# Kernel optimization log

Hardware: AMD Instinct MI355X
Metric: run time of the kernel (lower is better)

The kernel has to match this reference:

```python
import jax, jax.numpy as jnp
import numpy as np

UNITS = 32
ATT_WIDTH = 64


def setup_inputs() -> dict:
    key = jax.random.key(0)
    ks = jax.random.split(key, 4)
    B, T, F = 4, 1024, 256
    x = jax.random.normal(ks[0], (B, T, F), dtype=jnp.float32)
    Wt = jax.random.normal(ks[1], (F, UNITS), dtype=jnp.float32) * (1.0 / np.sqrt(F))
    Wx = jax.random.normal(ks[2], (F, UNITS), dtype=jnp.float32) * (1.0 / np.sqrt(F))
    bh = jnp.zeros((UNITS,), dtype=jnp.float32)
    Wa = jax.random.normal(ks[3], (UNITS, 1), dtype=jnp.float32) * (1.0 / np.sqrt(UNITS))
    ba = jnp.zeros((1,), dtype=jnp.float32)
    return {"x": x, "Wt": Wt, "Wx": Wx, "bh": bh, "Wa": Wa, "ba": ba}


def reference(x, Wt, Wx, bh, Wa, ba):
    # Additive (Bahdanau-style) self-attention emission:
    # h[b,t,s,u] = tanh(x[b,t] @ Wt + x[b,s] @ Wx + bh)
    q = jnp.einsum('btf,fu->btu', x, Wt)[:, :, None, :]   # [B,T,1,U]
    k = jnp.einsum('bsf,fu->bsu', x, Wx)[:, None, :, :]   # [B,1,T,U]
    h = jnp.tanh(q + k + bh)                               # [B,T,T,U]
    e = jnp.einsum('btsu,uo->bts', h, Wa) + ba[0]          # [B,T,T]

    # Local attention window (symmetric, width=ATT_WIDTH)
    T = x.shape[1]
    idx = jnp.arange(T)
    lower = idx - ATT_WIDTH // 2                           # [T]
    band = (lower[:, None] <= idx[None, :]) & (idx[None, :] < lower[:, None] + ATT_WIDTH)
    e = e - 10000.0 * (1.0 - band.astype(e.dtype))

    a = jax.nn.softmax(e, axis=-1)                         # [B,T,T]
    v = jnp.einsum('bts,bsf->btf', a, x)                   # [B,T,F]
    return v
```

## Files before the change

kernel.cpp:

```cpp
#include <hip/hip_runtime.h>
#include <math.h>

#define BB 4
#define TT 1024
#define FF 256
#define UU 32
#define HALF_W 32
#define WMAX 64

__device__ __forceinline__ float fast_tanh(float x) {
    float e = __expf(2.0f * x);
    return 1.0f - 2.0f / (e + 1.0f);
}

__global__ __launch_bounds__(256) void qk_kernel(
    const float* __restrict__ x, const float* __restrict__ Wt,
    const float* __restrict__ Wx, const float* __restrict__ bh,
    float* __restrict__ qbuf, float* __restrict__ kbuf) {
    int row0 = blockIdx.x * 4;
    int tid = threadIdx.x;
    __shared__ float xs[4][FF];
    {
        int r = tid >> 6;
        int c4 = tid & 63;
        ((float4*)xs[r])[c4] = ((const float4*)(x + (size_t)(row0 + r) * FF))[c4];
    }
    __syncthreads();
    int r = tid >> 6;
    int half = (tid >> 5) & 1;
    int u = tid & 31;
    const float* __restrict__ W = half ? Wx : Wt;
    const float* __restrict__ xr = xs[r];
    float acc = 0.f;
#pragma unroll 8
    for (int f = 0; f < FF; ++f)
        acc = fmaf(xr[f], W[f * UU + u], acc);
    int row = row0 + r;
    if (half == 0) qbuf[row * UU + u] = acc + bh[u];
    else           kbuf[row * UU + u] = acc;
}

__global__ __launch_bounds__(256) void attn_kernel(
    const float* __restrict__ x, const float* __restrict__ qbuf,
    const float* __restrict__ kbuf, const float* __restrict__ Wa,
    const float* __restrict__ ba, float* __restrict__ out) {
    int row = blockIdx.x;
    int t = row & (TT - 1);
    int b = row >> 10;
    int tid = threadIdx.x;
    int s0 = max(0, t - HALF_W);
    int s1 = min(TT, t + HALF_W);
    int W_ = s1 - s0;

    __shared__ float q_sh[UU];
    __shared__ float wa_sh[UU];
    __shared__ float e_sh[WMAX];
    __shared__ float a_sh[WMAX];

    if (tid < UU) {
        q_sh[tid]  = qbuf[row * UU + tid];
        wa_sh[tid] = Wa[tid];
    }
    __syncthreads();

    int sl = tid >> 2;
    int j  = tid & 3;
    float partial = 0.f;
    if (sl < W_) {
        const float4* krow = (const float4*)(kbuf + (size_t)(b * TT + s0 + sl) * UU + j * 8);
        float4 k0 = krow[0];
        float4 k1 = krow[1];
        int u = j * 8;
        partial  = fast_tanh(q_sh[u + 0] + k0.x) * wa_sh[u + 0];
        partial += fast_tanh(q_sh[u + 1] + k0.y) * wa_sh[u + 1];
        partial += fast_tanh(q_sh[u + 2] + k0.z) * wa_sh[u + 2];
        partial += fast_tanh(q_sh[u + 3] + k0.w) * wa_sh[u + 3];
        partial += fast_tanh(q_sh[u + 4] + k1.x) * wa_sh[u + 4];
        partial += fast_tanh(q_sh[u + 5] + k1.y) * wa_sh[u + 5];
        partial += fast_tanh(q_sh[u + 6] + k1.z) * wa_sh[u + 6];
        partial += fast_tanh(q_sh[u + 7] + k1.w) * wa_sh[u + 7];
    }
    partial += __shfl_xor(partial, 1);
    partial += __shfl_xor(partial, 2);
    if (j == 0) e_sh[sl] = (sl < W_) ? partial + ba[0] : -1e30f;
    __syncthreads();

    if (tid < 64) {
        float e = e_sh[tid];
        float m = e;
#pragma unroll
        for (int off = 1; off < 64; off <<= 1) m = fmaxf(m, __shfl_xor(m, off));
        float p = __expf(e - m);
        float sum = p;
#pragma unroll
        for (int off = 1; off < 64; off <<= 1) sum += __shfl_xor(sum, off);
        a_sh[tid] = p / sum;
    }
    __syncthreads();

    float acc = 0.f;
    const float* xb = x + (size_t)(b * TT + s0) * FF + tid;
#pragma unroll 4
    for (int k2 = 0; k2 < W_; ++k2)
        acc = fmaf(a_sh[k2], xb[(size_t)k2 * FF], acc);
    out[(size_t)row * FF + tid] = acc;
}

__global__ __launch_bounds__(256) void fused_kernel(
    const float* __restrict__ x, const float* __restrict__ Wt,
    const float* __restrict__ Wx, const float* __restrict__ bh,
    const float* __restrict__ Wa, const float* __restrict__ ba,
    float* __restrict__ out) {
    int row = blockIdx.x;
    int t = row & (TT - 1);
    int b = row >> 10;
    int tid = threadIdx.x;
    int s0 = max(0, t - HALF_W);
    int s1 = min(TT, t + HALF_W);
    int W_ = s1 - s0;

    __shared__ float ks[WMAX * UU];
    __shared__ float q_sh[UU];
    __shared__ float wa_sh[UU];
    __shared__ float e_sh[WMAX];
    __shared__ float a_sh[WMAX];

    if (tid < UU) {
        const float* xr = x + (size_t)row * FF;
        float acc = 0.f;
        for (int f = 0; f < FF; ++f) acc = fmaf(xr[f], Wt[f * UU + tid], acc);
        q_sh[tid]  = acc + bh[tid];
        wa_sh[tid] = Wa[tid];
    }
    for (int p = tid; p < W_ * UU; p += 256) {
        int sl = p >> 5, u = p & 31;
        const float* xr = x + (size_t)(b * TT + s0 + sl) * FF;
        float acc = 0.f;
        for (int f = 0; f < FF; ++f) acc = fmaf(xr[f], Wx[f * UU + u], acc);
        ks[p] = acc;
    }
    __syncthreads();

    int sl = tid >> 2;
    int j  = tid & 3;
    float partial = 0.f;
    if (sl < W_) {
#pragma unroll
        for (int uu = 0; uu < 8; ++uu) {
            int u = j * 8 + uu;
            partial += fast_tanh(q_sh[u] + ks[sl * UU + u]) * wa_sh[u];
        }
    }
    partial += __shfl_xor(partial, 1);
    partial += __shfl_xor(partial, 2);
    if (j == 0) e_sh[sl] = (sl < W_) ? partial + ba[0] : -1e30f;
    __syncthreads();

    if (tid < 64) {
        float e = e_sh[tid];
        float m = e;
#pragma unroll
        for (int off = 1; off < 64; off <<= 1) m = fmaxf(m, __shfl_xor(m, off));
        float p = __expf(e - m);
        float sum = p;
#pragma unroll
        for (int off = 1; off < 64; off <<= 1) sum += __shfl_xor(sum, off);
        a_sh[tid] = p / sum;
    }
    __syncthreads();

    float acc = 0.f;
    const float* xb = x + (size_t)(b * TT + s0) * FF + tid;
    for (int k2 = 0; k2 < W_; ++k2)
        acc = fmaf(a_sh[k2], xb[(size_t)k2 * FF], acc);
    out[(size_t)row * FF + tid] = acc;
}

extern "C" void kernel_launch(void* const* d_in, const int* in_sizes, int n_in,
                              void* d_out, int out_size, void* d_ws, size_t ws_size,
                              hipStream_t stream) {
    const float* x  = (const float*)d_in[0];
    const float* Wt = (const float*)d_in[1];
    const float* Wx = (const float*)d_in[2];
    const float* bh = (const float*)d_in[3];
    const float* Wa = (const float*)d_in[4];
    const float* ba = (const float*)d_in[5];
    float* out = (float*)d_out;

    const size_t need = (size_t)2 * BB * TT * UU * sizeof(float);
    if (ws_size >= need) {
        float* qbuf = (float*)d_ws;
        float* kbuf = qbuf + (size_t)BB * TT * UU;
        qk_kernel<<<BB * TT / 4, 256, 0, stream>>>(x, Wt, Wx, bh, qbuf, kbuf);
        attn_kernel<<<BB * TT, 256, 0, stream>>>(x, qbuf, kbuf, Wa, ba, out);
    } else {
        fused_kernel<<<BB * TT, 256, 0, stream>>>(x, Wt, Wx, bh, Wa, ba, out);
    }
}
```

Measured before the change: 91.96 us.

## Register-tile qk projection with 8 outputs per thread and split-K shuffles

Result: no change. 90.37 us (-1.7%).

```diff
diff --git a/kernel.cpp b/kernel.cpp
--- a/kernel.cpp
+++ b/kernel.cpp
@@ -7,6 +7,7 @@
 #define UU 32
 #define HALF_W 32
 #define WMAX 64
+#define RB 8
 
 __device__ __forceinline__ float fast_tanh(float x) {
     float e = __expf(2.0f * x);
@@ -17,27 +18,71 @@
     const float* __restrict__ x, const float* __restrict__ Wt,
     const float* __restrict__ Wx, const float* __restrict__ bh,
     float* __restrict__ qbuf, float* __restrict__ kbuf) {
-    int row0 = blockIdx.x * 4;
+    int row0 = blockIdx.x * RB;
     int tid = threadIdx.x;
-    __shared__ float xs[4][FF];
+    __shared__ float xs[RB][FF + 4];
     {
-        int r = tid >> 6;
-        int c4 = tid & 63;
-        ((float4*)xs[r])[c4] = ((const float4*)(x + (size_t)(row0 + r) * FF))[c4];
-    }
-    __syncthreads();
-    int r = tid >> 6;
-    int half = (tid >> 5) & 1;
-    int u = tid & 31;
+        const float4* src = (const float4*)(x + (size_t)row0 * FF);
+#pragma unroll
+        for (int i = 0; i < 2; ++i) {
+            int p = tid + i * 256;
+            int r = p >> 6;
+            int c = p & 63;
+            *(float4*)&xs[r][c * 4] = src[p];
+        }
+    }
+    __syncthreads();
+
+    int r    = tid >> 5;
+    int sub  = tid & 31;
+    int half = sub >> 4;
+    int fh   = (sub >> 2) & 3;
+    int ug   = (sub & 3) * 8;
     const float* __restrict__ W = half ? Wx : Wt;
     const float* __restrict__ xr = xs[r];
-    float acc = 0.f;
-#pragma unroll 8
-    for (int f = 0; f < FF; ++f)
-        acc = fmaf(xr[f], W[f * UU + u], acc);
-    int row = row0 + r;
-    if (half == 0) qbuf[row * UU + u] = acc + bh[u];
-    else           kbuf[row * UU + u] = acc;
+
+    float acc[8] = {0.f, 0.f, 0.f, 0.f, 0.f, 0.f, 0.f, 0.f};
+#pragma unroll 4
+    for (int it = 0; it < 16; ++it) {
+        int f = 4 * fh + 16 * it;
+        float4 x4 = *(const float4*)&xr[f];
+#pragma unroll
+        for (int j = 0; j < 4; ++j) {
+            const float4* wp = (const float4*)(W + (size_t)(f + j) * UU + ug);
+            float4 w0 = wp[0];
+            float4 w1 = wp[1];
+            float xv = (j == 0) ? x4.x : (j == 1) ? x4.y : (j == 2) ? x4.z : x4.w;
+            acc[0] = fmaf(xv, w0.x, acc[0]);
+            acc[1] = fmaf(xv, w0.y, acc[1]);
+            acc[2] = fmaf(xv, w0.z, acc[2]);
+            acc[3] = fmaf(xv, w0.w, acc[3]);
+            acc[4] = fmaf(xv, w1.x, acc[4]);
+            acc[5] = fmaf(xv, w1.y, acc[5]);
+            acc[6] = fmaf(xv, w1.z, acc[6]);
+            acc[7] = fmaf(xv, w1.w, acc[7]);
+        }
+    }
+#pragma unroll
+    for (int i = 0; i < 8; ++i) {
+        acc[i] += __shfl_xor(acc[i], 4);
+        acc[i] += __shfl_xor(acc[i], 8);
+    }
+    if (fh == 0) {
+        int row = row0 + r;
+        if (half == 0) {
+            float4 b0 = *(const float4*)&bh[ug];
+            float4 b1 = *(const float4*)&bh[ug + 4];
+            float4 o0 = {acc[0] + b0.x, acc[1] + b0.y, acc[2] + b0.z, acc[3] + b0.w};
+            float4 o1 = {acc[4] + b1.x, acc[5] + b1.y, acc[6] + b1.z, acc[7] + b1.w};
+            *(float4*)&qbuf[(size_t)row * UU + ug]     = o0;
+            *(float4*)&qbuf[(size_t)row * UU + ug + 4] = o1;
+        } else {
+            float4 o0 = {acc[0], acc[1], acc[2], acc[3]};
+            float4 o1 = {acc[4], acc[5], acc[6], acc[7]};
+            *(float4*)&kbuf[(size_t)row * UU + ug]     = o0;
+            *(float4*)&kbuf[(size_t)row * UU + ug + 4] = o1;
+        }
+    }
 }
 
 __global__ __launch_bounds__(256) void attn_kernel(
@@ -58,7 +103,7 @@
     __shared__ float a_sh[WMAX];
 
     if (tid < UU) {
-        q_sh[tid]  = qbuf[row * UU + tid];
+        q_sh[tid]  = qbuf[(size_t)row * UU + tid];
         wa_sh[tid] = Wa[tid];
     }
     __syncthreads();
@@ -191,7 +236,7 @@
     if (ws_size >= need) {
         float* qbuf = (float*)d_ws;
         float* kbuf = qbuf + (size_t)BB * TT * UU;
-        qk_kernel<<<BB * TT / 4, 256, 0, stream>>>(x, Wt, Wx, bh, qbuf, kbuf);
+        qk_kernel<<<BB * TT / RB, 256, 0, stream>>>(x, Wt, Wx, bh, qbuf, kbuf);
         attn_kernel<<<BB * TT, 256, 0, stream>>>(x, qbuf, kbuf, Wa, ba, out);
     } else {
         fused_kernel<<<BB * TT, 256, 0, stream>>>(x, Wt, Wx, bh, Wa, ba, out);
```
